# Kernel tuning notes

Measured on AMD Instinct MI355X. Metric: run time of the kernel, lower is better.

## Reference

```python
import jax, jax.numpy as jnp
import numpy as np
from jax import lax
import math

B, L, D = 2, 1024, 1024
H = 16
HD = D // H
DS = 16            # d_state
EXP = 2
DIN = EXP * D      # d_inner = 2048
DCONV = 4
DTR = math.ceil(D / 16)  # dt_rank = 64
EPS = 1e-5


def setup_inputs() -> dict:
    key = jax.random.key(0)
    ks = jax.random.split(key, 24)
    g = lambda i, shape, s=0.02: (jax.random.normal(ks[i], shape, dtype=jnp.float32) * s)
    A_log = jnp.log(jnp.tile(jnp.arange(1, DS + 1, dtype=jnp.float32)[None, :], (DIN, 1)))
    return {
        "x": jax.random.normal(ks[0], (B, L, D), dtype=jnp.float32),
        # MambaWrapper pre-norm
        "mnorm_w": jnp.ones((D,), jnp.float32), "mnorm_b": jnp.zeros((D,), jnp.float32),
        # MambaBlock params
        "in_proj_w": g(1, (2 * DIN, D)),
        "conv_w": g(2, (DIN, 1, DCONV), 0.1), "conv_b": jnp.zeros((DIN,), jnp.float32),
        "x_proj_w": g(3, (DTR + 2 * DS, DIN)),
        "dt_proj_w": g(4, (DIN, DTR)), "dt_proj_b": g(5, (DIN,), 0.01),
        "A_log": A_log, "D_skip": jnp.ones((DIN,), jnp.float32),
        "out_proj_w": g(6, (D, DIN)),
        # attention branch
        "norm1_w": jnp.ones((D,), jnp.float32), "norm1_b": jnp.zeros((D,), jnp.float32),
        "wqkv_w": g(7, (D + 2 * HD, D)), "wqkv_b": jnp.zeros((D + 2 * HD,), jnp.float32),
        "oattn_w": g(8, (D, D)), "oattn_b": jnp.zeros((D,), jnp.float32),
        # parallel fusion: Linear(2D->D) + LayerNorm
        "fuse_w": g(9, (D, 2 * D)), "fuse_b": jnp.zeros((D,), jnp.float32),
        "fln_w": jnp.ones((D,), jnp.float32), "fln_b": jnp.zeros((D,), jnp.float32),
    }


def _ln(x, w, b):
    m = x.mean(-1, keepdims=True)
    xc = x - m
    v = (xc * xc).mean(-1, keepdims=True)
    return xc * lax.rsqrt(v + EPS) * w + b


def _selective_scan(u, delta, A, Bm, Cm, D_skip):
    # u, delta: (b,l,din); A: (din,n); Bm,Cm: (b,l,n)
    dA = jnp.exp(delta[..., None] * A)                    # (b,l,din,n)
    dBu = delta[..., None] * Bm[:, :, None, :] * u[..., None]

    def step(h, inp):
        dA_t, dBu_t, C_t = inp                            # (b,din,n),(b,din,n),(b,n)
        h = dA_t * h + dBu_t
        y = jnp.einsum('bdn,bn->bd', h, C_t)
        return h, y

    h0 = jnp.zeros((u.shape[0], u.shape[2], A.shape[1]), u.dtype)
    _, ys = lax.scan(step, h0, (dA.transpose(1, 0, 2, 3), dBu.transpose(1, 0, 2, 3), Cm.transpose(1, 0, 2)))
    return ys.transpose(1, 0, 2) + u * D_skip             # (b,l,din)


def _mamba_branch(x, mnorm_w, mnorm_b, in_proj_w, conv_w, conv_b, x_proj_w,
                  dt_proj_w, dt_proj_b, A_log, D_skip, out_proj_w):
    xn = _ln(x, mnorm_w, mnorm_b)
    xr = xn @ in_proj_w.T                                 # (b,l,2*din)
    u, res = xr[..., :DIN], xr[..., DIN:]
    # depthwise causal conv1d (torch pads d_conv-1 both sides then slices [:l])
    uc = u.transpose(0, 2, 1)                             # (b,din,l)
    uc = lax.conv_general_dilated(uc, conv_w, (1,), [(DCONV - 1, 0)],
                                  dimension_numbers=('NCH', 'OIH', 'NCH'),
                                  feature_group_count=DIN) + conv_b[None, :, None]
    u = jax.nn.silu(uc.transpose(0, 2, 1))
    dbc = u @ x_proj_w.T                                  # (b,l,dtr+2n)
    delta = jax.nn.softplus(dbc[..., :DTR] @ dt_proj_w.T + dt_proj_b)
    Bm = dbc[..., DTR:DTR + DS]
    Cm = dbc[..., DTR + DS:]
    y = _selective_scan(u, delta, -jnp.exp(A_log), Bm, Cm, D_skip)
    y = y * jax.nn.silu(res)
    return (y @ out_proj_w.T) + x                         # dropout=identity (eval), +residual


def _mqa_branch(x, norm1_w, norm1_b, wqkv_w, wqkv_b, oattn_w, oattn_b):
    xn = _ln(x, norm1_w, norm1_b)
    qkv = xn @ wqkv_w.T + wqkv_b
    q = qkv[..., :D].reshape(B, L, H, HD)
    k = qkv[..., D:D + HD]                                # shared single K head (b,l,hd)
    v = qkv[..., D + HD:]
    scores = jnp.einsum('blhd,bsd->bhls', q, k) / math.sqrt(HD)
    causal = jnp.tril(jnp.ones((L, L), bool))
    scores = jnp.where(causal, scores, jnp.finfo(scores.dtype).min)
    attn = jax.nn.softmax(scores, axis=-1)
    o = jnp.einsum('bhls,bsd->blhd', attn, v).reshape(B, L, D)
    return x + (o @ oattn_w.T + oattn_b)


def reference(x, mnorm_w, mnorm_b, in_proj_w, conv_w, conv_b, x_proj_w,
              dt_proj_w, dt_proj_b, A_log, D_skip, out_proj_w,
              norm1_w, norm1_b, wqkv_w, wqkv_b, oattn_w, oattn_b,
              fuse_w, fuse_b, fln_w, fln_b):
    mamba_out = _mamba_branch(x, mnorm_w, mnorm_b, in_proj_w, conv_w, conv_b, x_proj_w,
                              dt_proj_w, dt_proj_b, A_log, D_skip, out_proj_w)
    attn_out = _mqa_branch(x, norm1_w, norm1_b, wqkv_w, wqkv_b, oattn_w, oattn_b)
    combined = jnp.concatenate([mamba_out, attn_out], axis=-1)
    fused = _ln(combined @ fuse_w.T + fuse_b, fln_w, fln_b)
    return fused
```

## Files before the change

### kernel.cpp

```cpp
#include <hip/hip_runtime.h>
#include <hip/hip_bf16.h>
#include <hip/hip_fp16.h>
#include <cstddef>


using bf16 = __hip_bfloat16;
using frag8 = __attribute__((ext_vector_type(8))) short;
using f32x4 = __attribute__((ext_vector_type(4))) float;

__device__ __forceinline__ float siluf(float x) { return x / (1.f + __expf(-x)); }

__device__ __forceinline__ int sigmode(const unsigned int* sig) {
    const unsigned int s = *sig;
    return s == 0x3F800000u ? 1 : (s == 0x3C003C00u ? 2 : 0);
}
__device__ __forceinline__ float ldx(const void* p, size_t i, int m) {
    if (m == 1) return reinterpret_cast<const float*>(p)[i];
    if (m == 2) return __half2float(reinterpret_cast<const __half*>(p)[i]);
    return __bfloat162float(reinterpret_cast<const bf16*>(p)[i]);
}

__device__ __forceinline__ void gload_lds16(const void* g, void* l) {
    __builtin_amdgcn_global_load_lds(
        (const __attribute__((address_space(1))) unsigned int*)g,
        (__attribute__((address_space(3))) unsigned int*)l, 16, 0, 0);
}

__global__ void sentinel_kernel(float* out, float code) {
    if (threadIdx.x == 0) out[0] = code;
}

__global__ __launch_bounds__(256) void wconv_kernel(const void* __restrict__ W, size_t off,
                                                    bf16* __restrict__ dst, int total8,
                                                    const unsigned int* __restrict__ sig) {
    const int g = blockIdx.x * 256 + threadIdx.x;
    if (g >= total8) return;
    const int md = sigmode(sig);
    const size_t i0 = off + (size_t)g * 8;
    union { bf16 h[8]; uint4 v; } u;
    if (md == 0) {
        u.v = *reinterpret_cast<const uint4*>((const bf16*)W + i0);
    } else {
#pragma unroll
        for (int j = 0; j < 8; ++j) u.h[j] = __float2bfloat16(ldx(W, i0 + j, md));
    }
    *reinterpret_cast<uint4*>(dst + (size_t)g * 8) = u.v;
}

__global__ __launch_bounds__(256) void wconv2_kernel(
    const void* __restrict__ W1, bf16* __restrict__ dst1, int total8_1,
    const void* __restrict__ W2, bf16* __restrict__ dst2, int total8_2,
    const unsigned int* __restrict__ sig) {
    const int g = blockIdx.x * 256 + threadIdx.x;
    const int md = sigmode(sig);
    const void* W;
    bf16* dst;
    int gg;
    if (g < total8_1) { W = W1; dst = dst1; gg = g; }
    else if (g < total8_1 + total8_2) { W = W2; dst = dst2; gg = g - total8_1; }
    else return;
    const size_t i0 = (size_t)gg * 8;
    union { bf16 h[8]; uint4 v; } u;
    if (md == 0) {
        u.v = *reinterpret_cast<const uint4*>((const bf16*)W + i0);
    } else {
#pragma unroll
        for (int j = 0; j < 8; ++j) u.h[j] = __float2bfloat16(ldx(W, i0 + j, md));
    }
    *reinterpret_cast<uint4*>(dst + i0) = u.v;
}

template <typename TO>
__global__ __launch_bounds__(256) void ln_kernel(
    const void* __restrict__ x, int x_from_in,
    const void* __restrict__ w, const void* __restrict__ b,
    const unsigned int* __restrict__ sig, TO* __restrict__ out) {
    const int md = sigmode(sig);
    const int xm = x_from_in ? md : 0;
    const int row = blockIdx.x;
    const int tid = threadIdx.x;
    __shared__ float red[256];
    const size_t base = (size_t)row * 1024;
    float v[4];
    float s = 0.f;
#pragma unroll
    for (int i = 0; i < 4; ++i) { v[i] = ldx(x, base + tid + i * 256, xm); s += v[i]; }
    red[tid] = s;
    __syncthreads();
    for (int st = 128; st > 0; st >>= 1) {
        if (tid < st) red[tid] += red[tid + st];
        __syncthreads();
    }
    const float mean = red[0] * (1.f / 1024.f);
    __syncthreads();
    float s2 = 0.f;
#pragma unroll
    for (int i = 0; i < 4; ++i) { v[i] -= mean; s2 += v[i] * v[i]; }
    red[tid] = s2;
    __syncthreads();
    for (int st = 128; st > 0; st >>= 1) {
        if (tid < st) red[tid] += red[tid + st];
        __syncthreads();
    }
    const float inv = rsqrtf(red[0] * (1.f / 1024.f) + 1e-5f);
#pragma unroll
    for (int i = 0; i < 4; ++i) {
        const int d = tid + i * 256;
        const float r = v[i] * inv * ldx(w, d, md) + ldx(b, d, md);
        if constexpr (sizeof(TO) == 4) out[base + d] = r;
        else out[base + d] = __float2bfloat16(r);
    }
}

template <int BM, int BN>
__global__ __launch_bounds__(256) void mfma_gemm(
    const bf16* __restrict__ A1, const bf16* __restrict__ A2, int KA1, int lda,
    const bf16* __restrict__ Wb,
    const void* __restrict__ bias,
    const void* __restrict__ resid, int ldr,
    bf16* __restrict__ C, int ldc,
    int K, int Nbound, int act, const unsigned int* __restrict__ sig,
    bf16* __restrict__ vt) {
    constexpr int NFR = (BN == 64) ? 1 : ((BM == 128) ? 4 : 2);
    const int md = sigmode(sig);
    __shared__ __align__(16) bf16 Als[BM * 32];
    __shared__ __align__(16) bf16 Wls[BN * 32];
    const int tid = threadIdx.x;
    const int lane = tid & 63;
    const int w = tid >> 6;
    const int arow = (BM == 128) ? ((w >> 1) * 64) : 0;
    const int bcol = (BN == 64) ? (w * 16) : ((BM == 128) ? ((w & 1) * 64) : (w * 32));
    const int m0 = blockIdx.y * BM;
    const int n0 = blockIdx.x * BN;
    f32x4 acc[4][NFR];
#pragma unroll
    for (int i = 0; i < 4; ++i)
#pragma unroll
        for (int j = 0; j < NFR; ++j) acc[i][j] = {0.f, 0.f, 0.f, 0.f};
    const int fm = lane & 15;
    const int fq = lane >> 4;
    for (int kk = 0; kk < K; kk += 32) {
        if constexpr (BM == 128) {
#pragma unroll
            for (int i = 0; i < 2; ++i) {
                const int chunk = i * 256 + tid;
                const int r = chunk >> 2, q = chunk & 3;
                const int gk = kk + q * 8;
                const bf16* srcA = (A2 != nullptr && gk >= KA1)
                    ? (A2 + (size_t)(m0 + r) * lda + (gk - KA1))
                    : (A1 + (size_t)(m0 + r) * lda + gk);
                gload_lds16(srcA, (char*)Als + (size_t)(i * 256 + w * 64) * 16);
            }
        } else {
            const int r = tid >> 2, q = tid & 3;
            const int gk = kk + q * 8;
            const bf16* srcA = (A2 != nullptr && gk >= KA1)
                ? (A2 + (size_t)(m0 + r) * lda + (gk - KA1))
                : (A1 + (size_t)(m0 + r) * lda + gk);
            gload_lds16(srcA, (char*)Als + (size_t)(w * 64) * 16);
        }
#pragma unroll
        for (int i = 0; i < (BN == 64 ? 1 : 2); ++i) {
            const int chunk = i * 256 + tid;
            const int r = chunk >> 2, q = chunk & 3;
            const bf16* srcW = Wb + (size_t)(n0 + r) * K + kk + q * 8;
            gload_lds16(srcW, (char*)Wls + (size_t)(i * 256 + w * 64) * 16);
        }
        __syncthreads();
        frag8 af[4], bfr[NFR];
#pragma unroll
        for (int ms = 0; ms < 4; ++ms)
            af[ms] = *reinterpret_cast<const frag8*>(&Als[(size_t)(arow + ms * 16 + fm) * 32 + fq * 8]);
#pragma unroll
        for (int ns = 0; ns < NFR; ++ns)
            bfr[ns] = *reinterpret_cast<const frag8*>(&Wls[(size_t)(bcol + ns * 16 + fm) * 32 + fq * 8]);
#pragma unroll
        for (int ms = 0; ms < 4; ++ms)
#pragma unroll
            for (int ns = 0; ns < NFR; ++ns)
                acc[ms][ns] = __builtin_amdgcn_mfma_f32_16x16x32_bf16(af[ms], bfr[ns], acc[ms][ns], 0, 0, 0);
        __syncthreads();
    }
#pragma unroll
    for (int ms = 0; ms < 4; ++ms) {
#pragma unroll
        for (int r = 0; r < 4; ++r) {
            const int m = m0 + arow + ms * 16 + fq * 4 + r;
#pragma unroll
            for (int ns = 0; ns < NFR; ++ns) {
                const int n = n0 + bcol + ns * 16 + fm;
                if (n < Nbound) {
                    float v = acc[ms][ns][r];
                    if (bias) v += ldx(bias, n, md);
                    if (resid) v += ldx(resid, (size_t)m * ldr + n, md);
                    if (act == 1) v = (v > 20.f) ? v : log1pf(expf(v));
                    const bf16 hv = __float2bfloat16(v);
                    C[(size_t)m * ldc + n] = hv;
                    if (vt != nullptr && n >= 1088) {
                        vt[((size_t)((m >> 10) * 64 + (n - 1088))) * 1024 + (m & 1023)] = hv;
                    }
                }
            }
        }
    }
}

__global__ __launch_bounds__(256) void conv_silu_kernel(
    const bf16* __restrict__ u0, int us, const void* __restrict__ cw,
    const void* __restrict__ cb, const unsigned int* __restrict__ sig,
    bf16* __restrict__ u) {
    const int md = sigmode(sig);
    const int idx = blockIdx.x * 256 + threadIdx.x;
    const int c8 = (idx & 255) * 8;
    const int bl = idx >> 8;
    const int l = bl & 1023;
    float acc[8];
#pragma unroll
    for (int i = 0; i < 8; ++i) acc[i] = ldx(cb, c8 + i, md);
#pragma unroll
    for (int k = 0; k < 4; ++k) {
        const int ls = l - 3 + k;
        if (ls >= 0) {
            union { frag8 v; bf16 h[8]; } uin;
            uin.v = *reinterpret_cast<const frag8*>(u0 + (size_t)(bl - 3 + k) * us + c8);
#pragma unroll
            for (int i = 0; i < 8; ++i)
                acc[i] += __bfloat162float(uin.h[i]) * ldx(cw, (c8 + i) * 4 + k, md);
        }
    }
    union { frag8 v; bf16 h[8]; } uo;
#pragma unroll
    for (int i = 0; i < 8; ++i) uo.h[i] = __float2bfloat16(siluf(acc[i]));
    *reinterpret_cast<frag8*>(u + (size_t)bl * 2048 + c8) = uo.v;
}

__global__ __launch_bounds__(512) void scan_kernel(
    bf16* __restrict__ delta_y, const bf16* __restrict__ u,
    const bf16* __restrict__ dbc, const bf16* __restrict__ res,
    const void* __restrict__ A_log, const void* __restrict__ D_skip,
    const unsigned int* __restrict__ sig) {
    constexpr int DYS = 4096;
    constexpr int US  = 2048;
    constexpr int BS  = 96;
    constexpr int PRS = 20;
    constexpr int PJS = 168;
    const int md = sigmode(sig);
    const int n = threadIdx.x & 15;
    const int j = threadIdx.x >> 4;
    const int bx = blockIdx.x;
    const int c = ((bx & 7) << 8) | (bx >> 3);
    const int b = blockIdx.y;
    __shared__ float Ac[32 * 17], Hc[32 * 17], h0s[32 * 17];
    __shared__ __align__(16) float P[32 * PJS];
    __shared__ __align__(16) bf16 Dcol[1024], Ucol[1024];
    const float acoef = -expf(ldx(A_log, c * 16 + n, md));
    const float dsk = ldx(D_skip, c, md);
    const int t0 = j * 32;
    const int bt0 = b * 1024 + t0;

    {
        const int tid = threadIdx.x;
#pragma unroll
        for (int rr = 0; rr < 2; ++rr) {
            const int t = tid + rr * 512;
            Dcol[t] = delta_y[(size_t)(b * 1024 + t) * DYS + c];
            Ucol[t] = u[(size_t)(b * 1024 + t) * US + c];
        }
    }
    __syncthreads();

    float dv[32];

    {
        const bf16* pb = dbc + (size_t)bt0 * BS + 64 + n;
        float hloc = 0.f, aprod = 1.f;
#pragma unroll
        for (int g = 0; g < 2; ++g) {
            bf16 Bv[16];
#pragma unroll
            for (int k = 0; k < 16; ++k) Bv[k] = pb[(size_t)(g * 16 + k) * BS];
#pragma unroll
            for (int k = 0; k < 16; ++k) {
                const int tt = g * 16 + k;
                const float dlt = __bfloat162float(Dcol[t0 + tt]);
                const float ut = __bfloat162float(Ucol[t0 + tt]);
                const float Bn = __bfloat162float(Bv[k]);
                const float a = __expf(dlt * acoef);
                const float dBu = dlt * Bn * ut;
                dv[tt] = dBu;
                hloc = a * hloc + dBu;
                aprod *= a;
            }
        }
        Ac[j * 17 + n] = aprod;
        Hc[j * 17 + n] = hloc;
    }
    __syncthreads();
    if (threadIdx.x < 16) {
        float e = 0.f;
        for (int jj = 0; jj < 32; ++jj) {
            h0s[jj * 17 + threadIdx.x] = e;
            e = Ac[jj * 17 + threadIdx.x] * e + Hc[jj * 17 + threadIdx.x];
        }
    }
    __syncthreads();

    float h = h0s[j * 17 + n];
    float psum[2];
    float* Pj = &P[j * PJS];
    {
        const bf16* pc = dbc + (size_t)bt0 * BS + 80 + n;
        const int nq = n >> 3;
        const int nr = n & 7;
#pragma unroll
        for (int q = 0; q < 4; ++q) {
            bf16 Cv[8];
#pragma unroll
            for (int k = 0; k < 8; ++k) Cv[k] = pc[(size_t)(q * 8 + k) * BS];
#pragma unroll
            for (int k = 0; k < 8; ++k) {
                const int tt = q * 8 + k;
                const float dlt = __bfloat162float(Dcol[t0 + tt]);
                const float a = __expf(dlt * acoef);
                h = a * h + dv[tt];
                Pj[k * PRS + n] = h * __bfloat162float(Cv[k]);
            }
            if (nq == (q & 1)) {
                const f32x4* pr = reinterpret_cast<const f32x4*>(&Pj[nr * PRS]);
                float s = 0.f;
#pragma unroll
                for (int v = 0; v < 4; ++v) {
                    const f32x4 q4 = pr[v];
                    s += q4[0] + q4[1] + q4[2] + q4[3];
                }
                psum[q >> 1] = s;
            }
        }
    }
#pragma unroll
    for (int half = 0; half < 2; ++half) {
        const int tl = t0 + half * 16 + n;
        const size_t id = (size_t)(b * 1024 + tl) * DYS + c;
        const float ut = __bfloat162float(Ucol[tl]);
        const float r = __bfloat162float(res[id]);
        delta_y[id] = __float2bfloat16((psum[half] + ut * dsk) * siluf(r));
    }
}

__global__ __launch_bounds__(128) void attn_mfma(const bf16* __restrict__ qkv,
                                                 const bf16* __restrict__ Vt,
                                                 bf16* __restrict__ o) {
    const int tid = threadIdx.x;
    const int lane = tid & 63;
    const int wv = tid >> 6;
    const int fm = lane & 15, quad = lane >> 4;
    const int qt = blockIdx.x, h = blockIdx.y, b = blockIdx.z;
    __shared__ __align__(16) bf16 Pls[2][64][72];
    __shared__ float Ols[64][68];
    __shared__ float Mst[64], Lst[64];

    frag8 qf[4][2];
#pragma unroll
    for (int ms = 0; ms < 4; ++ms)
#pragma unroll
        for (int kq = 0; kq < 2; ++kq)
            qf[ms][kq] = *reinterpret_cast<const frag8*>(
                qkv + ((size_t)(b * 1024 + qt * 64 + ms * 16 + fm)) * 1152 + h * 64 + kq * 32 + quad * 8);

    float mrun[4][4], lrun[4][4];
    f32x4 acco[4][4];
#pragma unroll
    for (int ms = 0; ms < 4; ++ms)
#pragma unroll
        for (int r = 0; r < 4; ++r) { mrun[ms][r] = -1.0e30f; lrun[ms][r] = 0.f; }
#pragma unroll
    for (int ms = 0; ms < 4; ++ms)
#pragma unroll
        for (int nd = 0; nd < 4; ++nd) acco[ms][nd] = {0.f, 0.f, 0.f, 0.f};

    for (int st = wv; st <= qt; st += 2) {
        f32x4 accs[4][4];
#pragma unroll
        for (int ms = 0; ms < 4; ++ms)
#pragma unroll
            for (int ns = 0; ns < 4; ++ns) accs[ms][ns] = {0.f, 0.f, 0.f, 0.f};
        __builtin_amdgcn_s_setprio(1);
#pragma unroll
        for (int ns = 0; ns < 4; ++ns) {
            frag8 kf[2];
#pragma unroll
            for (int kq = 0; kq < 2; ++kq)
                kf[kq] = *reinterpret_cast<const frag8*>(
                    qkv + ((size_t)(b * 1024 + st * 64 + ns * 16 + fm)) * 1152 + 1024 + kq * 32 + quad * 8);
#pragma unroll
            for (int ms = 0; ms < 4; ++ms) {
                accs[ms][ns] = __builtin_amdgcn_mfma_f32_16x16x32_bf16(qf[ms][0], kf[0], accs[ms][ns], 0, 0, 0);
                accs[ms][ns] = __builtin_amdgcn_mfma_f32_16x16x32_bf16(qf[ms][1], kf[1], accs[ms][ns], 0, 0, 0);
            }
        }
        __builtin_amdgcn_s_setprio(0);
        const bool diag = (st == qt);
#pragma unroll
        for (int ms = 0; ms < 4; ++ms) {
            float alpha[4];
#pragma unroll
            for (int r = 0; r < 4; ++r) {
                const int ql = ms * 16 + quad * 4 + r;
                float sv[4];
#pragma unroll
                for (int ns = 0; ns < 4; ++ns) {
                    const int sl = ns * 16 + fm;
                    sv[ns] = (!diag || sl <= ql) ? accs[ms][ns][r] * 0.125f : -1.0e30f;
                }
                float mloc = fmaxf(fmaxf(sv[0], sv[1]), fmaxf(sv[2], sv[3]));
                mloc = fmaxf(mloc, __shfl_xor(mloc, 1));
                mloc = fmaxf(mloc, __shfl_xor(mloc, 2));
                mloc = fmaxf(mloc, __shfl_xor(mloc, 4));
                mloc = fmaxf(mloc, __shfl_xor(mloc, 8));
                const float mnew = fmaxf(mrun[ms][r], mloc);
                alpha[r] = __expf(mrun[ms][r] - mnew);
                float rs = 0.f;
#pragma unroll
                for (int ns = 0; ns < 4; ++ns) {
                    const float p = __expf(sv[ns] - mnew);
                    rs += p;
                    Pls[wv][ms * 16 + quad * 4 + r][ns * 16 + fm] = __float2bfloat16(p);
                }
                rs += __shfl_xor(rs, 1);
                rs += __shfl_xor(rs, 2);
                rs += __shfl_xor(rs, 4);
                rs += __shfl_xor(rs, 8);
                lrun[ms][r] = lrun[ms][r] * alpha[r] + rs;
                mrun[ms][r] = mnew;
            }
#pragma unroll
            for (int nd = 0; nd < 4; ++nd)
#pragma unroll
                for (int r = 0; r < 4; ++r) acco[ms][nd][r] *= alpha[r];
        }
        frag8 pf[4][2];
#pragma unroll
        for (int ms = 0; ms < 4; ++ms)
#pragma unroll
            for (int ks = 0; ks < 2; ++ks)
                pf[ms][ks] = *reinterpret_cast<const frag8*>(&Pls[wv][ms * 16 + fm][ks * 32 + quad * 8]);
        __builtin_amdgcn_s_setprio(1);
#pragma unroll
        for (int nd = 0; nd < 4; ++nd) {
            frag8 vf[2];
#pragma unroll
            for (int ks = 0; ks < 2; ++ks)
                vf[ks] = *reinterpret_cast<const frag8*>(
                    Vt + ((size_t)b * 64 + nd * 16 + fm) * 1024 + st * 64 + ks * 32 + quad * 8);
#pragma unroll
            for (int ms = 0; ms < 4; ++ms) {
                acco[ms][nd] = __builtin_amdgcn_mfma_f32_16x16x32_bf16(pf[ms][0], vf[0], acco[ms][nd], 0, 0, 0);
                acco[ms][nd] = __builtin_amdgcn_mfma_f32_16x16x32_bf16(pf[ms][1], vf[1], acco[ms][nd], 0, 0, 0);
            }
        }
        __builtin_amdgcn_s_setprio(0);
    }

    __syncthreads();
    if (wv == 1) {
#pragma unroll
        for (int ms = 0; ms < 4; ++ms)
#pragma unroll
            for (int r = 0; r < 4; ++r) {
                const int q = ms * 16 + quad * 4 + r;
                Mst[q] = mrun[ms][r];
                Lst[q] = lrun[ms][r];
#pragma unroll
                for (int nd = 0; nd < 4; ++nd)
                    Ols[q][nd * 16 + fm] = acco[ms][nd][r];
            }
    }
    __syncthreads();
    if (wv == 0) {
#pragma unroll
        for (int ms = 0; ms < 4; ++ms)
#pragma unroll
            for (int r = 0; r < 4; ++r) {
                const int q = ms * 16 + quad * 4 + r;
                const float m1 = Mst[q], l1 = Lst[q];
                const float M = fmaxf(mrun[ms][r], m1);
                const float a0 = __expf(mrun[ms][r] - M);
                const float a1 = __expf(m1 - M);
                const float L = lrun[ms][r] * a0 + l1 * a1;
                const float inv = 1.f / fmaxf(L, 1e-30f);
                const size_t row = (size_t)(b * 1024 + qt * 64 + q);
#pragma unroll
                for (int nd = 0; nd < 4; ++nd)
                    o[row * 1024 + h * 64 + nd * 16 + fm] =
                        __float2bfloat16((acco[ms][nd][r] * a0 + Ols[q][nd * 16 + fm] * a1) * inv);
            }
    }
}

extern "C" void kernel_launch(void* const* d_in, const int* in_sizes, int n_in,
                              void* d_out, int out_size, void* d_ws, size_t ws_size,
                              hipStream_t stream) {
    float* out = (float*)d_out;

    static const int kExp[22] = {
        2097152, 1024, 1024, 4194304, 8192, 2048, 196608, 131072, 2048, 32768,
        2048, 2097152, 1024, 1024, 1179648, 1152, 1048576, 1024, 2097152, 1024,
        1024, 1024};
    const size_t kNeedBytes = 29360128;
    float code = 0.f;
    if (n_in != 22) code = 65536.f * (32 + (n_in & 31));
    else if (out_size != 2097152) code = 65536.f * 200.f;
    else {
        for (int i = 0; i < 22; ++i)
            if (in_sizes[i] != kExp[i]) { code = 65536.f * (64 + i); break; }
        if (code == 0.f && ws_size < kNeedBytes)
            code = 65536.f * (128.f + (float)(ws_size >> 20));
    }
    if (code != 0.f) {
        sentinel_kernel<<<dim3(1), dim3(64), 0, stream>>>(out, code);
        return;
    }

    const unsigned int* sig = (const unsigned int*)d_in[1];

    bf16* ws = (bf16*)d_ws;
    bf16* Aslot = ws;
    bf16* Bslot = ws + 2097152;
    bf16* Cslot = ws + 6291456;
    bf16* Dslot = ws + 10485760;
    bf16* dbc    = Aslot;
    bf16* xprojW = Aslot + 262144;
    bf16* dtW    = Aslot + 524288;
    bf16* u0res  = Bslot;
    bf16* mambaOut = Dslot;
    bf16* DsHi = Dslot + 2097152;
    bf16* BsHi = Bslot + 2097152;
    bf16* Vt   = Bslot + 1572864;

    const dim3 b256(256);
    const int NOSPLIT = 1 << 30;
    const int NB = 1 << 30;

    ln_kernel<bf16><<<dim3(2048), b256, 0, stream>>>(d_in[0], 1, d_in[1], d_in[2], sig, Aslot);
    wconv_kernel<<<dim3(2048), b256, 0, stream>>>(d_in[3], 0, Dslot, 524288, sig);
    mfma_gemm<128, 128><<<dim3(32, 16), b256, 0, stream>>>(Aslot, nullptr, NOSPLIT, 1024,
        Dslot, nullptr, nullptr, 0, u0res, 4096, 1024, NB, 0, sig, nullptr);
    conv_silu_kernel<<<dim3(2048), b256, 0, stream>>>(u0res, 4096, d_in[4], d_in[5], sig, Dslot);
    wconv2_kernel<<<dim3(160), b256, 0, stream>>>(d_in[6], xprojW, 24576, d_in[7], dtW, 16384, sig);
    mfma_gemm<128, 128><<<dim3(1, 16), b256, 0, stream>>>(Dslot, nullptr, NOSPLIT, 2048,
        xprojW, nullptr, nullptr, 0, dbc, 96, 2048, 96, 0, sig, nullptr);
    mfma_gemm<64, 128><<<dim3(16, 32), b256, 0, stream>>>(dbc, nullptr, NOSPLIT, 96,
        dtW, d_in[8], nullptr, 0, u0res, 4096, 64, NB, 1, sig, nullptr);
    scan_kernel<<<dim3(2048, 2), dim3(512), 0, stream>>>(u0res, Dslot, dbc, u0res + 2048,
        d_in[9], d_in[10], sig);
    wconv_kernel<<<dim3(1024), b256, 0, stream>>>(d_in[11], 0, DsHi, 262144, sig);
    mfma_gemm<64, 64><<<dim3(16, 32), b256, 0, stream>>>(u0res, nullptr, NOSPLIT, 4096,
        DsHi, nullptr, d_in[0], 1024, mambaOut, 1024, 2048, NB, 0, sig, nullptr);

    ln_kernel<bf16><<<dim3(2048), b256, 0, stream>>>(d_in[0], 1, d_in[12], d_in[13], sig, Aslot);
    wconv_kernel<<<dim3(576), b256, 0, stream>>>(d_in[14], 0, Bslot, 147456, sig);
    mfma_gemm<64, 64><<<dim3(18, 32), b256, 0, stream>>>(Aslot, nullptr, NOSPLIT, 1024,
        Bslot, d_in[15], nullptr, 0, Cslot, 1152, 1024, NB, 0, sig, Vt);
    attn_mfma<<<dim3(16, 16, 2), dim3(128), 0, stream>>>(Cslot, Vt, DsHi);
    wconv_kernel<<<dim3(512), b256, 0, stream>>>(d_in[16], 0, Bslot, 131072, sig);
    mfma_gemm<64, 64><<<dim3(16, 32), b256, 0, stream>>>(DsHi, nullptr, NOSPLIT, 1024,
        Bslot, d_in[17], d_in[0], 1024, BsHi, 1024, 1024, NB, 0, sig, nullptr);

    wconv_kernel<<<dim3(1024), b256, 0, stream>>>(d_in[18], 0, Cslot, 262144, sig);
    mfma_gemm<64, 64><<<dim3(16, 32), b256, 0, stream>>>(mambaOut, BsHi, 1024, 1024,
        Cslot, d_in[19], nullptr, 0, Aslot, 1024, 2048, NB, 0, sig, nullptr);
    ln_kernel<float><<<dim3(2048), b256, 0, stream>>>(Aslot, 0, d_in[20], d_in[21], sig, out);
}
```

Baseline: 623.0 us.

## Split attention KV loop across four waves with tree merge; add scan occupancy hint

The attention kernel now runs four waves per block instead of two. Each wave handles every fourth key tile, and the partial softmax states are combined in a two-level merge through shared memory, with the P and O staging buffers aliased to keep LDS small. This targets the serial KV loop and the low wave count of causal attention, at the cost of extra syncs and merge work. The scan kernel also gets a min-blocks launch-bounds hint to limit register use and raise occupancy.

```diff
diff --git a/kernel.cpp b/kernel.cpp
--- a/kernel.cpp
+++ b/kernel.cpp
@@ -234,7 +234,7 @@
     *reinterpret_cast<frag8*>(u + (size_t)bl * 2048 + c8) = uo.v;
 }
 
-__global__ __launch_bounds__(512) void scan_kernel(
+__global__ __launch_bounds__(512, 6) void scan_kernel(
     bf16* __restrict__ delta_y, const bf16* __restrict__ u,
     const bf16* __restrict__ dbc, const bf16* __restrict__ res,
     const void* __restrict__ A_log, const void* __restrict__ D_skip,
@@ -347,7 +347,7 @@
     }
 }
 
-__global__ __launch_bounds__(128) void attn_mfma(const bf16* __restrict__ qkv,
+__global__ __launch_bounds__(256) void attn_mfma(const bf16* __restrict__ qkv,
                                                  const bf16* __restrict__ Vt,
                                                  bf16* __restrict__ o) {
     const int tid = threadIdx.x;
@@ -355,9 +355,10 @@
     const int wv = tid >> 6;
     const int fm = lane & 15, quad = lane >> 4;
     const int qt = blockIdx.x, h = blockIdx.y, b = blockIdx.z;
-    __shared__ __align__(16) bf16 Pls[2][64][72];
-    __shared__ float Ols[64][68];
-    __shared__ float Mst[64], Lst[64];
+    __shared__ __align__(16) char shbuf[4 * 64 * 72 * sizeof(bf16)];
+    bf16 (*Pls)[64][72] = reinterpret_cast<bf16 (*)[64][72]>(shbuf);
+    float (*Ols)[64][68] = reinterpret_cast<float (*)[64][68]>(shbuf);
+    __shared__ float Mst[2][64], Lst[2][64];
 
     frag8 qf[4][2];
 #pragma unroll
@@ -378,7 +379,7 @@
 #pragma unroll
         for (int nd = 0; nd < 4; ++nd) acco[ms][nd] = {0.f, 0.f, 0.f, 0.f};
 
-    for (int st = wv; st <= qt; st += 2) {
+    for (int st = wv; st <= qt; st += 4) {
         f32x4 accs[4][4];
 #pragma unroll
         for (int ms = 0; ms < 4; ++ms)
@@ -462,27 +463,60 @@
     }
 
     __syncthreads();
-    if (wv == 1) {
+    if (wv >= 2) {
+        const int s = wv - 2;
 #pragma unroll
         for (int ms = 0; ms < 4; ++ms)
 #pragma unroll
             for (int r = 0; r < 4; ++r) {
                 const int q = ms * 16 + quad * 4 + r;
-                Mst[q] = mrun[ms][r];
-                Lst[q] = lrun[ms][r];
+                Mst[s][q] = mrun[ms][r];
+                Lst[s][q] = lrun[ms][r];
 #pragma unroll
                 for (int nd = 0; nd < 4; ++nd)
-                    Ols[q][nd * 16 + fm] = acco[ms][nd][r];
-            }
-    }
-    __syncthreads();
-    if (wv == 0) {
+                    Ols[s][q][nd * 16 + fm] = acco[ms][nd][r];
+            }
+    }
+    __syncthreads();
+    if (wv < 2) {
 #pragma unroll
         for (int ms = 0; ms < 4; ++ms)
 #pragma unroll
             for (int r = 0; r < 4; ++r) {
                 const int q = ms * 16 + quad * 4 + r;
-                const float m1 = Mst[q], l1 = Lst[q];
+                const float m1 = Mst[wv][q], l1 = Lst[wv][q];
+                const float M = fmaxf(mrun[ms][r], m1);
+                const float a0 = __expf(mrun[ms][r] - M);
+                const float a1 = __expf(m1 - M);
+                lrun[ms][r] = lrun[ms][r] * a0 + l1 * a1;
+                mrun[ms][r] = M;
+#pragma unroll
+                for (int nd = 0; nd < 4; ++nd)
+                    acco[ms][nd][r] = acco[ms][nd][r] * a0 + Ols[wv][q][nd * 16 + fm] * a1;
+            }
+    }
+    __syncthreads();
+    if (wv == 1) {
+#pragma unroll
+        for (int ms = 0; ms < 4; ++ms)
+#pragma unroll
+            for (int r = 0; r < 4; ++r) {
+                const int q = ms * 16 + quad * 4 + r;
+                Mst[0][q] = mrun[ms][r];
+                Lst[0][q] = lrun[ms][r];
+#pragma unroll
+                for (int nd = 0; nd < 4; ++nd)
+                    Ols[0][q][nd * 16 + fm] = acco[ms][nd][r];
+            }
+    }
+    __syncthreads();
+    if (wv == 0) {
+#pragma unroll
+        for (int ms = 0; ms < 4; ++ms)
+#pragma unroll
+            for (int r = 0; r < 4; ++r) {
+                const int q = ms * 16 + quad * 4 + r;
+                const float m1 = Mst[0][q], l1 = Lst[0][q];
                 const float M = fmaxf(mrun[ms][r], m1);
                 const float a0 = __expf(mrun[ms][r] - M);
                 const float a1 = __expf(m1 - M);
@@ -492,7 +526,7 @@
 #pragma unroll
                 for (int nd = 0; nd < 4; ++nd)
                     o[row * 1024 + h * 64 + nd * 16 + fm] =
-                        __float2bfloat16((acco[ms][nd][r] * a0 + Ols[q][nd * 16 + fm] * a1) * inv);
+                        __float2bfloat16((acco[ms][nd][r] * a0 + Ols[0][q][nd * 16 + fm] * a1) * inv);
             }
     }
 }
@@ -561,7 +595,7 @@
     wconv_kernel<<<dim3(576), b256, 0, stream>>>(d_in[14], 0, Bslot, 147456, sig);
     mfma_gemm<64, 64><<<dim3(18, 32), b256, 0, stream>>>(Aslot, nullptr, NOSPLIT, 1024,
         Bslot, d_in[15], nullptr, 0, Cslot, 1152, 1024, NB, 0, sig, Vt);
-    attn_mfma<<<dim3(16, 16, 2), dim3(128), 0, stream>>>(Cslot, Vt, DsHi);
+    attn_mfma<<<dim3(16, 16, 2), dim3(256), 0, stream>>>(Cslot, Vt, DsHi);
     wconv_kernel<<<dim3(512), b256, 0, stream>>>(d_in[16], 0, Bslot, 131072, sig);
     mfma_gemm<64, 64><<<dim3(16, 32), b256, 0, stream>>>(DsHi, nullptr, NOSPLIT, 1024,
         Bslot, d_in[17], d_in[0], 1024, BsHi, 1024, 1024, NB, 0, sig, nullptr);
```

Result: faster. 607.8 us (-2.4%).
